# Kernel tuning notes

Hardware: AMD Instinct MI355X
Metric: run time of the kernel (lower is better)

Reference implementation:

```python
import jax, jax.numpy as jnp
import numpy as np

IM_H, IM_W = 240, 320
ENV_R, ENV_C = 120, 160
ENV_H, ENV_W = 8, 16
GRID = 8
NGRIDS = 6 * GRID * GRID  # 384


def _normalize(v, axis, eps=1e-6):
    return v / (jnp.linalg.norm(v, axis=axis, keepdims=True) + eps)


def setup_inputs() -> dict:
    key = jax.random.key(0)
    k1, k2, k3, k4 = jax.random.split(key, 4)
    B = 2
    normalPred = jax.random.normal(k1, (B, 3, IM_H, IM_W), dtype=jnp.float32)
    # positive depth in [0.5, 5.0] so z = -depth passes the z < -0.1 mask mostly
    depthPred = jax.random.uniform(k2, (B, IM_H, IM_W), dtype=jnp.float32, minval=0.5, maxval=5.0)
    envmapsPredImage = jax.random.uniform(k3, (B, 3, ENV_R, ENV_C, ENV_H, ENV_W), dtype=jnp.float32)
    # intrinsics must have cx = W/2, cy = H/2 (module asserts f_W_scale == f_H_scale)
    cam_K = jnp.tile(jnp.array([[300.0, 0.0, IM_W / 2.0],
                                [0.0, 300.0, IM_H / 2.0],
                                [0.0, 0.0, 1.0]], dtype=jnp.float32)[None], (B, 1, 1))
    # grid-cell centers of the 6 layout faces in LightNet coords (normally from get_grid_centers)
    verts_center_lightNet = jax.random.normal(k4, (B, 6, GRID, GRID, 3), dtype=jnp.float32) * 3.0
    return {"normalPred": normalPred, "depthPred": depthPred,
            "envmapsPredImage": envmapsPredImage, "cam_K": cam_K,
            "verts_center_lightNet": verts_center_lightNet}


def _forward(normalPred, depthPred, envmapsPredImage, cam_K, verts_center_lightNet):
    B = depthPred.shape[0]
    dt = depthPred.dtype
    # ---- back-project per-pixel 3D points from depth + intrinsics ----
    u0, v0 = IM_W / 2.0, IM_H / 2.0
    vv, uu = jnp.meshgrid(jnp.arange(IM_H, dtype=dt), jnp.arange(IM_W, dtype=dt), indexing='ij')
    f_pix = (cam_K[:, 0, 0] * (IM_W / 2.0) / cam_K[:, 0, 2]).reshape(B, 1, 1)
    z = -depthPred
    x = -(uu - u0) / f_pix * z
    y = (vv - v0) / f_pix * z
    points = jnp.stack([x, y, z], axis=1)  # [B,3,IM_H,IM_W]

    # ---- renderingLayer.forwardEnv (if_normal_only): per-pixel local frame at env res ----
    r = IM_H // ENV_R  # = IM_W // ENV_C = 2
    n = normalPred.reshape(B, 3, ENV_R, r, ENV_C, r).mean(axis=(3, 5))
    normal = _normalize(n, axis=1)                              # [B,3,eR,eC]
    up = jnp.array([0.0, 1.0, 0.0], dtype=dt).reshape(1, 3, 1, 1)
    camyProj = (up * normal).sum(axis=1, keepdims=True) * normal
    camy = _normalize(up - camyProj, axis=1)
    camx = -_normalize(jnp.cross(camy, normal, axis=1), axis=1)

    # ---- accu_light ----
    pts_s = points[:, :, ::r, ::r].transpose(0, 2, 3, 1)        # [B,eR,eC,3]
    mask = pts_s[..., 2] < -0.1                                 # [B,eR,eC]
    p_t = verts_center_lightNet.reshape(B, NGRIDS, 1, 1, 3)
    vec_to_t = p_t - pts_s[:, None]                             # [B,G,eR,eC,3]

    # A columns = [camx, camy, normal]; invert per pixel
    A = jnp.stack([camx.transpose(0, 2, 3, 1),
                   camy.transpose(0, 2, 3, 1),
                   normal.transpose(0, 2, 3, 1)], axis=-1)      # [B,eR,eC,3,3]
    A = A + 1e-6 * jnp.eye(3, dtype=dt)
    invA = jnp.linalg.inv(A)

    l_local = jnp.einsum('bhwij,bghwj->bghwi', invA, vec_to_t)  # [B,G,eR,eC,3]
    l_local = _normalize(l_local, axis=-1)
    cos_theta = l_local[..., 2]
    theta = jnp.arccos(cos_theta)
    sin_t = jnp.sin(theta) + 1e-6
    phi = jnp.arctan2(l_local[..., 1] / sin_t, l_local[..., 0] / sin_t)
    az = (phi / np.pi / 2.0 + 0.5) * ENV_W                      # [B,G,eR,eC]
    el = theta / np.pi * 2.0 * ENV_H

    # grid_sample(bilinear, padding='border', align_corners=False) on per-pixel 8x16 envmaps
    # normalized coord -> pixel coord: (uv/size*2-1 + 1)*size/2 - 0.5 = uv - 0.5
    az_f = jnp.clip(az.transpose(0, 2, 3, 1).reshape(-1, NGRIDS) - 0.5, 0.0, ENV_W - 1.0)
    el_f = jnp.clip(el.transpose(0, 2, 3, 1).reshape(-1, NGRIDS) - 0.5, 0.0, ENV_H - 1.0)
    x0 = jnp.floor(az_f); fx = az_f - x0
    y0 = jnp.floor(el_f); fy = el_f - y0
    x0i = x0.astype(jnp.int32); x1i = jnp.minimum(x0i + 1, ENV_W - 1)
    y0i = y0.astype(jnp.int32); y1i = jnp.minimum(y0i + 1, ENV_H - 1)

    env_flat = envmapsPredImage.transpose(0, 2, 3, 1, 4, 5).reshape(-1, 3, ENV_H * ENV_W)  # [Npix,3,128]

    def gather(yi, xi):
        idx = (yi * ENV_W + xi)[:, None, :]                     # [Npix,1,G]
        return jnp.take_along_axis(env_flat, idx, axis=2)       # [Npix,3,G]

    fx_ = fx[:, None, :]; fy_ = fy[:, None, :]
    val = (gather(y0i, x0i) * (1 - fx_) * (1 - fy_) +
           gather(y0i, x1i) * fx_ * (1 - fy_) +
           gather(y1i, x0i) * (1 - fx_) * fy_ +
           gather(y1i, x1i) * fx_ * fy_)                        # [Npix,3,G]

    env_acc = val.reshape(B, ENV_R, ENV_C, 3, NGRIDS).transpose(0, 3, 4, 1, 2)  # [B,3,G,eR,eC]
    mask_e = mask.astype(dt)[:, None, None]                     # [B,1,1,eR,eC]
    env_acc = env_acc * mask_e
    env_mean = (env_acc.sum((-1, -2)) / (mask_e.sum((-1, -2)) + 1e-6)).transpose(0, 2, 1)  # [B,G,3]
    return env_acc, env_mean, points, mask, vec_to_t


def reference(normalPred, depthPred, envmapsPredImage, cam_K, verts_center_lightNet):
    return _forward(normalPred, depthPred, envmapsPredImage, cam_K, verts_center_lightNet)
```

## Files before the change

kernel.cpp:

```cpp
#include <hip/hip_runtime.h>
#include <math.h>

namespace {

constexpr int IMH = 240, IMW = 320;
constexpr int ER = 120, EC = 160, EH = 8, EW = 16;
constexpr int NG = 384;
constexpr int NPIX = ER * EC;
constexpr int NB = 2;
constexpr int NTAP = EH * EW;

constexpr size_t ACC_N    = (size_t)NB * 3 * NG * NPIX;
constexpr size_t OFF_ACC  = 0;
constexpr size_t OFF_MEAN = OFF_ACC + ACC_N;
constexpr size_t MEAN_N   = (size_t)NB * NG * 3;
constexpr size_t OFF_PTS  = OFF_MEAN + MEAN_N;
constexpr size_t PTS_N    = (size_t)NB * 3 * IMH * IMW;
constexpr size_t OFF_MASK = OFF_PTS + PTS_N;
constexpr size_t MASK_N   = (size_t)NB * NPIX;
constexpr size_t OFF_VEC  = OFF_MASK + MASK_N;

constexpr int TPX   = 32;
constexpr int GLN   = 8;
constexpr int GIT   = NG / GLN;
constexpr int TILES = NPIX / TPX;
constexpr int LROW  = 132;

constexpr size_t WS_S     = (size_t)NB * NPIX;
constexpr size_t WS_INVA  = 0;
constexpr size_t WS_PTS   = WS_INVA + 9 * WS_S;
constexpr size_t WS_PART  = WS_PTS + 3 * WS_S;
constexpr size_t PART_N   = (size_t)NB * NG * 3 * TILES;
constexpr size_t WS_CNT_HI = WS_PART + PART_N;
constexpr size_t WS_CNT_LO = WS_PART;
constexpr size_t WS_NEED_HI = (WS_CNT_HI + NB) * 4;

__device__ __forceinline__ float fpix_of(const float* K, int b) {
    return K[b * 9 + 0] * (IMW * 0.5f) / K[b * 9 + 2];
}

__device__ __forceinline__ unsigned bf16r(float f) {
    unsigned b = __float_as_uint(f);
    return (b + 0x7FFFu + ((b >> 16) & 1u)) >> 16;
}
__device__ __forceinline__ float bfload(unsigned short u) {
    return __uint_as_float((unsigned)u << 16);
}

template <int CTRL, int RMASK>
__device__ __forceinline__ float dpp_add(float s) {
    int t = __builtin_amdgcn_update_dpp(0, __float_as_int(s), CTRL, RMASK, 0xf, true);
    return s + __int_as_float(t);
}
__device__ __forceinline__ float hw_sum(float s) {
    s = dpp_add<0x111, 0xf>(s);
    s = dpp_add<0x112, 0xf>(s);
    s = dpp_add<0x114, 0xf>(s);
    s = dpp_add<0x118, 0xf>(s);
    s = dpp_add<0x142, 0xa>(s);
    return s;
}

__device__ __forceinline__ float acos_el(float x) {
    float ax = fminf(fabsf(x), 1.0f);
    float p  = fmaf(fmaf(fmaf(-0.09538315f, ax, 0.37820512f), ax, -1.08021632f),
                    ax, 7.99996873f);
    float r  = sqrtf(1.0f - ax) * p;
    return (x >= 0.0f) ? r : 16.0f - r;
}

__device__ __forceinline__ float atan2_az(float y, float x) {
    float ay = fabsf(y), ax = fabsf(x);
    float mn = fminf(ax, ay), mx = fmaxf(ax, ay);
    float a  = mn * __builtin_amdgcn_rcpf(fmaxf(mx, 1e-37f));
    float s  = a * a;
    float r  = a * fmaf(s, fmaf(s, fmaf(s, fmaf(s, 0.05305631f, -0.21677864f),
                                        0.45872349f), -0.84104627f), 2.54613763f);
    if (ay > ax) r = 4.0f - r;
    if (x < 0.0f) r = 8.0f - r;
    return fmaf(copysignf(1.0f, y), r, 8.0f);
}

__global__ void k_points_zero(const float* __restrict__ depth,
                              const float* __restrict__ K,
                              float* __restrict__ out,
                              float* __restrict__ ws, size_t cnt_off) {
    int idx = blockIdx.x * 256 + threadIdx.x;
    if (blockIdx.x == 0 && threadIdx.x < NB) ws[cnt_off + threadIdx.x] = 0.0f;
    if (idx >= NB * IMH * IMW) return;
    int b  = idx / (IMH * IMW);
    int pp = idx - b * (IMH * IMW);
    int v  = pp / IMW;
    int u  = pp - v * IMW;
    float fp = fpix_of(K, b);
    float z  = -depth[idx];
    float x  = -(((float)u - IMW * 0.5f) / fp) * z;
    float y  =  (((float)v - IMH * 0.5f) / fp) * z;
    float* P = out + OFF_PTS + (size_t)b * 3 * IMH * IMW;
    P[pp]                 = x;
    P[pp + IMH * IMW]     = y;
    P[pp + 2 * IMH * IMW] = z;
}

__global__ void k_prep(const float* __restrict__ normal,
                       const float* __restrict__ depth,
                       const float* __restrict__ K,
                       float* __restrict__ out,
                       float* __restrict__ ws, size_t cnt_off) {
    int idx = blockIdx.x * 256 + threadIdx.x;
    if (idx >= NB * NPIX) return;
    int b   = idx / NPIX;
    int pix = idx - b * NPIX;
    int h   = pix / EC;
    int w   = pix - h * EC;
    int v = 2 * h, u = 2 * w;

    float fp = fpix_of(K, b);
    float z  = -depth[(size_t)b * IMH * IMW + (size_t)v * IMW + u];
    float px = -(((float)u - 160.0f) / fp) * z;
    float py =  (((float)v - 120.0f) / fp) * z;

    ws[WS_PTS + 0 * WS_S + idx] = px;
    ws[WS_PTS + 1 * WS_S + idx] = py;
    ws[WS_PTS + 2 * WS_S + idx] = z;

    float m = (z < -0.1f) ? 1.0f : 0.0f;
    out[OFF_MASK + idx] = m;
    float cm = m;
    for (int off = 32; off > 0; off >>= 1) cm += __shfl_down(cm, off);
    if ((threadIdx.x & 63) == 0) atomicAdd(&ws[cnt_off + b], cm);

    float n[3];
#pragma unroll
    for (int c = 0; c < 3; ++c) {
        const float* Nc = normal + ((size_t)(b * 3 + c) * IMH + v) * IMW + u;
        n[c] = 0.25f * (Nc[0] + Nc[1] + Nc[IMW] + Nc[IMW + 1]);
    }
    float nl = sqrtf(n[0]*n[0] + n[1]*n[1] + n[2]*n[2]) + 1e-6f;
    float nx = n[0] / nl, ny = n[1] / nl, nz = n[2] / nl;

    float t0 = -ny * nx, t1 = 1.0f - ny * ny, t2 = -ny * nz;
    float tl = sqrtf(t0*t0 + t1*t1 + t2*t2) + 1e-6f;
    float cy0 = t0 / tl, cy1 = t1 / tl, cy2 = t2 / tl;

    float cr0 = cy1 * nz - cy2 * ny;
    float cr1 = cy2 * nx - cy0 * nz;
    float cr2 = cy0 * ny - cy1 * nx;
    float cl = sqrtf(cr0*cr0 + cr1*cr1 + cr2*cr2) + 1e-6f;
    float cx0 = -cr0 / cl, cx1 = -cr1 / cl, cx2 = -cr2 / cl;

    float a00 = cx0 + 1e-6f, a01 = cy0,         a02 = nx;
    float a10 = cx1,         a11 = cy1 + 1e-6f, a12 = ny;
    float a20 = cx2,         a21 = cy2,         a22 = nz + 1e-6f;

    float c00 =  a11 * a22 - a12 * a21;
    float c01 = -(a10 * a22 - a12 * a20);
    float c02 =  a10 * a21 - a11 * a20;
    float det = a00 * c00 + a01 * c01 + a02 * c02;
    float id  = 1.0f / det;

    ws[WS_INVA + 0 * WS_S + idx] = c00 * id;
    ws[WS_INVA + 1 * WS_S + idx] = (a02 * a21 - a01 * a22) * id;
    ws[WS_INVA + 2 * WS_S + idx] = (a01 * a12 - a02 * a11) * id;
    ws[WS_INVA + 3 * WS_S + idx] = c01 * id;
    ws[WS_INVA + 4 * WS_S + idx] = (a00 * a22 - a02 * a20) * id;
    ws[WS_INVA + 5 * WS_S + idx] = (a02 * a10 - a00 * a12) * id;
    ws[WS_INVA + 6 * WS_S + idx] = c02 * id;
    ws[WS_INVA + 7 * WS_S + idx] = (a01 * a20 - a00 * a21) * id;
    ws[WS_INVA + 8 * WS_S + idx] = (a00 * a11 - a01 * a10) * id;
}

template <bool WP>
__global__ void __launch_bounds__(256) k_main(const float* __restrict__ env,
                       const float* __restrict__ verts,
                       float* __restrict__ out,
                       float* __restrict__ ws) {
    __shared__ unsigned       lds01[TPX * LROW];
    __shared__ unsigned short lds2 [TPX * LROW];

    int blk  = blockIdx.x;
    int b    = blk / TILES;
    int tile = blk - b * TILES;
    int px0  = tile * TPX;
    int t    = threadIdx.x;

    {
        const float* ebase = env + (size_t)b * 3 * NPIX * NTAP + (size_t)px0 * NTAP;
#pragma unroll
        for (int it2 = 0; it2 < 4; ++it2) {
            int idx2 = it2 * 256 + t;
            int ppx  = idx2 >> 5;
            int tq   = idx2 & 31;
            const float* p0 = ebase + (size_t)ppx * NTAP + tq * 4;
            float4 c0 = *(const float4*)(p0);
            float4 c1 = *(const float4*)(p0 + (size_t)NPIX * NTAP);
            float4 c2 = *(const float4*)(p0 + (size_t)2 * NPIX * NTAP);
            uint4 pk;
            pk.x = bf16r(c0.x) | (bf16r(c1.x) << 16);
            pk.y = bf16r(c0.y) | (bf16r(c1.y) << 16);
            pk.z = bf16r(c0.z) | (bf16r(c1.z) << 16);
            pk.w = bf16r(c0.w) | (bf16r(c1.w) << 16);
            *(uint4*)(&lds01[ppx * LROW + tq * 4]) = pk;
            ushort4 s4;
            s4.x = (unsigned short)bf16r(c2.x);
            s4.y = (unsigned short)bf16r(c2.y);
            s4.z = (unsigned short)bf16r(c2.z);
            s4.w = (unsigned short)bf16r(c2.w);
            *(ushort4*)(&lds2[ppx * LROW + tq * 4]) = s4;
        }
    }
    __syncthreads();

    int px_l  = t & 31;
    int glane = t >> 5;
    int pix   = px0 + px_l;
    int bp    = b * NPIX + pix;
    int row   = px_l * LROW;

    float px = ws[WS_PTS + 0 * WS_S + bp];
    float py = ws[WS_PTS + 1 * WS_S + bp];
    float pz = ws[WS_PTS + 2 * WS_S + bp];
    float i00 = ws[WS_INVA + 0 * WS_S + bp];
    float i01 = ws[WS_INVA + 1 * WS_S + bp];
    float i02 = ws[WS_INVA + 2 * WS_S + bp];
    float i10 = ws[WS_INVA + 3 * WS_S + bp];
    float i11 = ws[WS_INVA + 4 * WS_S + bp];
    float i12 = ws[WS_INVA + 5 * WS_S + bp];
    float i20 = ws[WS_INVA + 6 * WS_S + bp];
    float i21 = ws[WS_INVA + 7 * WS_S + bp];
    float i22 = ws[WS_INVA + 8 * WS_S + bp];
    float m = (pz < -0.1f) ? 1.0f : 0.0f;

    int g0 = glane * GIT;
    const float* vp = verts + ((size_t)b * NG + g0) * 3;
    float* pA0 = out + OFF_ACC + ((size_t)(b * 3 + 0) * NG + g0) * NPIX + pix;
    float* pA1 = out + OFF_ACC + ((size_t)(b * 3 + 1) * NG + g0) * NPIX + pix;
    float* pA2 = out + OFF_ACC + ((size_t)(b * 3 + 2) * NG + g0) * NPIX + pix;
    float* pV  = out + OFF_VEC + (((size_t)b * NG + g0) * NPIX + pix) * 3;
    float* pP  = ws + WS_PART + ((size_t)(b * NG + g0) * 3) * TILES + tile;

#pragma unroll 2
    for (int it = 0; it < GIT; ++it) {
        float vx = vp[0] - px, vy = vp[1] - py, vz = vp[2] - pz;
        pV[0] = vx; pV[1] = vy; pV[2] = vz;

        float l0 = i00 * vx + i01 * vy + i02 * vz;
        float l1 = i10 * vx + i11 * vy + i12 * vz;
        float l2 = i20 * vx + i21 * vy + i22 * vz;
        float nl = sqrtf(l0*l0 + l1*l1 + l2*l2) + 1e-6f;
        float l2n = l2 * __builtin_amdgcn_rcpf(nl);

        float el = acos_el(l2n);
        float az = atan2_az(l1, l0);

        float azf = __builtin_amdgcn_fmed3f(az - 0.5f, 0.0f, 15.0f);
        float elf = __builtin_amdgcn_fmed3f(el - 0.5f, 0.0f, 7.0f);
        float x0 = floorf(azf), y0 = floorf(elf);
        float fx = azf - x0,    fy = elf - y0;
        int x0i = (int)x0, y0i = (int)y0;
        int x1i = min(x0i + 1, 15);
        int y1i = min(y0i + 1, 7);

        float w00 = (1.0f - fx) * (1.0f - fy);
        float w01 = fx * (1.0f - fy);
        float w10 = (1.0f - fx) * fy;
        float w11 = fx * fy;

        int a00 = row + (y0i << 4) + x0i;
        int a01 = row + (y0i << 4) + x1i;
        int a10 = row + (y1i << 4) + x0i;
        int a11 = row + (y1i << 4) + x1i;

        unsigned q00 = lds01[a00], q01 = lds01[a01];
        unsigned q10 = lds01[a10], q11 = lds01[a11];

        float v0 = (__uint_as_float(q00 << 16) * w00 + __uint_as_float(q01 << 16) * w01 +
                    __uint_as_float(q10 << 16) * w10 + __uint_as_float(q11 << 16) * w11) * m;
        float v1 = (__uint_as_float(q00 & 0xFFFF0000u) * w00 + __uint_as_float(q01 & 0xFFFF0000u) * w01 +
                    __uint_as_float(q10 & 0xFFFF0000u) * w10 + __uint_as_float(q11 & 0xFFFF0000u) * w11) * m;
        float v2 = (bfload(lds2[a00]) * w00 + bfload(lds2[a01]) * w01 +
                    bfload(lds2[a10]) * w10 + bfload(lds2[a11]) * w11) * m;

        *pA0 = v0; *pA1 = v1; *pA2 = v2;

        if constexpr (WP) {
            float s0 = hw_sum(v0);
            float s1 = hw_sum(v1);
            float s2 = hw_sum(v2);
            if ((t & 31) == 31) {
                pP[0 * TILES] = s0;
                pP[1 * TILES] = s1;
                pP[2 * TILES] = s2;
            }
            pP += 3 * TILES;
        }

        vp  += 3;
        pV  += (size_t)NPIX * 3;
        pA0 += NPIX; pA1 += NPIX; pA2 += NPIX;
    }
}

__global__ void k_psum(float* __restrict__ out, const float* __restrict__ ws,
                       size_t cnt_off) {
    int r = blockIdx.x;
    int l = threadIdx.x;
    const float* p = ws + WS_PART + (size_t)r * TILES;
    float s = 0.0f;
    for (int i = l; i < TILES; i += 64) s += p[i];
#pragma unroll
    for (int off = 32; off > 0; off >>= 1) s += __shfl_down(s, off);
    if (l == 0) {
        int b = r / (NG * 3);
        out[OFF_MEAN + r] = s / (ws[cnt_off + b] + 1e-6f);
    }
}

__global__ void k_mean2(float* __restrict__ out, const float* __restrict__ ws,
                        size_t cnt_off) {
    __shared__ float wsum[4];
    int blk = blockIdx.x;
    int b   = blk / (3 * NG);
    int t   = threadIdx.x;

    const float4* r4 = (const float4*)(out + OFF_ACC + (size_t)blk * NPIX);
    float s = 0.0f;
    for (int i = t; i < NPIX / 4; i += 256) {
        float4 v = r4[i];
        s += v.x + v.y + v.z + v.w;
    }
    for (int off = 32; off > 0; off >>= 1) s += __shfl_down(s, off);
    if ((t & 63) == 0) wsum[t >> 6] = s;
    __syncthreads();
    if (t == 0) {
        int rc = blk - b * 3 * NG;
        int c  = rc / NG;
        int g  = rc - c * NG;
        float tot = wsum[0] + wsum[1] + wsum[2] + wsum[3];
        out[OFF_MEAN + ((size_t)b * NG + g) * 3 + c] = tot / (ws[cnt_off + b] + 1e-6f);
    }
}

}

extern "C" void kernel_launch(void* const* d_in, const int* in_sizes, int n_in,
                              void* d_out, int out_size, void* d_ws, size_t ws_size,
                              hipStream_t stream) {
    (void)in_sizes; (void)n_in; (void)out_size;
    const float* normalPred = (const float*)d_in[0];
    const float* depthPred  = (const float*)d_in[1];
    const float* env        = (const float*)d_in[2];
    const float* K          = (const float*)d_in[3];
    const float* verts      = (const float*)d_in[4];
    float* out = (float*)d_out;
    float* ws  = (float*)d_ws;

    const bool big = ws_size >= WS_NEED_HI;
    const size_t cnt_off = big ? WS_CNT_HI : WS_CNT_LO;

    k_points_zero<<<(NB * IMH * IMW + 255) / 256, 256, 0, stream>>>(depthPred, K, out, ws, cnt_off);
    k_prep<<<(NB * NPIX + 255) / 256, 256, 0, stream>>>(normalPred, depthPred, K, out, ws, cnt_off);
    if (big) {
        k_main<true><<<NB * TILES, 256, 0, stream>>>(env, verts, out, ws);
        k_psum<<<NB * NG * 3, 64, 0, stream>>>(out, ws, cnt_off);
    } else {
        k_main<false><<<NB * TILES, 256, 0, stream>>>(env, verts, out, ws);
        k_mean2<<<NB * 3 * NG, 256, 0, stream>>>(out, ws, cnt_off);
    }
}
```

Baseline: 125.1 us.

## Split vec_to_t output into separate coalesced float4 kernel and pad LDS rows

Moves the writing of the vec_to_t output out of the main env-sampling kernel into a dedicated kernel that writes contiguous float4 chunks. The old loop made strided 3-float scalar stores per pixel, which coalesce poorly. The LDS row stride for the packed channel-0/1 buffer also changes from 132 to 129 to cut bank conflicts during the random bilinear gathers. The cost is an extra launch and a second pass that re-reads points and verts, and the 129 stride forces scalar LDS writes in the staging phase.

```diff
diff --git a/kernel.cpp b/kernel.cpp
--- a/kernel.cpp
+++ b/kernel.cpp
@@ -24,7 +24,12 @@
 constexpr int GLN   = 8;
 constexpr int GIT   = NG / GLN;
 constexpr int TILES = NPIX / TPX;
-constexpr int LROW  = 132;
+constexpr int LR01  = 129;
+constexpr int LR2   = 132;
+
+constexpr int F4_PER_G = NPIX * 3 / 4;
+constexpr int F4_PER_B = NG * F4_PER_G;
+constexpr int VBLK     = NB * F4_PER_B / 1024;
 
 constexpr size_t WS_S     = (size_t)NB * NPIX;
 constexpr size_t WS_INVA  = 0;
@@ -170,13 +175,39 @@
     ws[WS_INVA + 8 * WS_S + idx] = (a00 * a11 - a01 * a10) * id;
 }
 
+__global__ void __launch_bounds__(256) k_vec(const float* __restrict__ verts,
+                                             float* __restrict__ out,
+                                             const float* __restrict__ ws) {
+#pragma unroll
+    for (int it = 0; it < 4; ++it) {
+        int f4i = (blockIdx.x * 4 + it) * 256 + threadIdx.x;
+        int b   = f4i / F4_PER_B;
+        int r4  = f4i - b * F4_PER_B;
+        int g   = r4 / F4_PER_G;
+        int rr  = (r4 - g * F4_PER_G) * 4;
+        const float* vv = verts + ((size_t)b * NG + g) * 3;
+        float v0 = vv[0], v1 = vv[1], v2 = vv[2];
+        const float* pb = ws + WS_PTS + (size_t)b * NPIX;
+        float4 o;
+#pragma unroll
+        for (int j = 0; j < 4; ++j) {
+            int rj  = rr + j;
+            int pxj = rj / 3;
+            int cj  = rj - 3 * pxj;
+            float vc = (cj == 0) ? v0 : ((cj == 1) ? v1 : v2);
+            (&o.x)[j] = vc - pb[(size_t)cj * WS_S + pxj];
+        }
+        *(float4*)(out + OFF_VEC + (size_t)f4i * 4) = o;
+    }
+}
+
 template <bool WP>
-__global__ void __launch_bounds__(256) k_main(const float* __restrict__ env,
+__global__ void __launch_bounds__(256) k_env(const float* __restrict__ env,
                        const float* __restrict__ verts,
                        float* __restrict__ out,
                        float* __restrict__ ws) {
-    __shared__ unsigned       lds01[TPX * LROW];
-    __shared__ unsigned short lds2 [TPX * LROW];
+    __shared__ unsigned       lds01[TPX * LR01];
+    __shared__ unsigned short lds2 [TPX * LR2];
 
     int blk  = blockIdx.x;
     int b    = blk / TILES;
@@ -195,18 +226,17 @@
             float4 c0 = *(const float4*)(p0);
             float4 c1 = *(const float4*)(p0 + (size_t)NPIX * NTAP);
             float4 c2 = *(const float4*)(p0 + (size_t)2 * NPIX * NTAP);
-            uint4 pk;
-            pk.x = bf16r(c0.x) | (bf16r(c1.x) << 16);
-            pk.y = bf16r(c0.y) | (bf16r(c1.y) << 16);
-            pk.z = bf16r(c0.z) | (bf16r(c1.z) << 16);
-            pk.w = bf16r(c0.w) | (bf16r(c1.w) << 16);
-            *(uint4*)(&lds01[ppx * LROW + tq * 4]) = pk;
+#pragma unroll
+            for (int k = 0; k < 4; ++k) {
+                lds01[ppx * LR01 + tq * 4 + k] =
+                    bf16r((&c0.x)[k]) | (bf16r((&c1.x)[k]) << 16);
+            }
             ushort4 s4;
             s4.x = (unsigned short)bf16r(c2.x);
             s4.y = (unsigned short)bf16r(c2.y);
             s4.z = (unsigned short)bf16r(c2.z);
             s4.w = (unsigned short)bf16r(c2.w);
-            *(ushort4*)(&lds2[ppx * LROW + tq * 4]) = s4;
+            *(ushort4*)(&lds2[ppx * LR2 + tq * 4]) = s4;
         }
     }
     __syncthreads();
@@ -215,7 +245,8 @@
     int glane = t >> 5;
     int pix   = px0 + px_l;
     int bp    = b * NPIX + pix;
-    int row   = px_l * LROW;
+    int row1  = px_l * LR01;
+    int row2  = px_l * LR2;
 
     float px = ws[WS_PTS + 0 * WS_S + bp];
     float py = ws[WS_PTS + 1 * WS_S + bp];
@@ -236,13 +267,11 @@
     float* pA0 = out + OFF_ACC + ((size_t)(b * 3 + 0) * NG + g0) * NPIX + pix;
     float* pA1 = out + OFF_ACC + ((size_t)(b * 3 + 1) * NG + g0) * NPIX + pix;
     float* pA2 = out + OFF_ACC + ((size_t)(b * 3 + 2) * NG + g0) * NPIX + pix;
-    float* pV  = out + OFF_VEC + (((size_t)b * NG + g0) * NPIX + pix) * 3;
     float* pP  = ws + WS_PART + ((size_t)(b * NG + g0) * 3) * TILES + tile;
 
 #pragma unroll 2
     for (int it = 0; it < GIT; ++it) {
         float vx = vp[0] - px, vy = vp[1] - py, vz = vp[2] - pz;
-        pV[0] = vx; pV[1] = vy; pV[2] = vz;
 
         float l0 = i00 * vx + i01 * vy + i02 * vz;
         float l1 = i10 * vx + i11 * vy + i12 * vz;
@@ -266,20 +295,20 @@
         float w10 = (1.0f - fx) * fy;
         float w11 = fx * fy;
 
-        int a00 = row + (y0i << 4) + x0i;
-        int a01 = row + (y0i << 4) + x1i;
-        int a10 = row + (y1i << 4) + x0i;
-        int a11 = row + (y1i << 4) + x1i;
-
-        unsigned q00 = lds01[a00], q01 = lds01[a01];
-        unsigned q10 = lds01[a10], q11 = lds01[a11];
+        int t00 = (y0i << 4) + x0i;
+        int t01 = (y0i << 4) + x1i;
+        int t10 = (y1i << 4) + x0i;
+        int t11 = (y1i << 4) + x1i;
+
+        unsigned q00 = lds01[row1 + t00], q01 = lds01[row1 + t01];
+        unsigned q10 = lds01[row1 + t10], q11 = lds01[row1 + t11];
 
         float v0 = (__uint_as_float(q00 << 16) * w00 + __uint_as_float(q01 << 16) * w01 +
                     __uint_as_float(q10 << 16) * w10 + __uint_as_float(q11 << 16) * w11) * m;
         float v1 = (__uint_as_float(q00 & 0xFFFF0000u) * w00 + __uint_as_float(q01 & 0xFFFF0000u) * w01 +
                     __uint_as_float(q10 & 0xFFFF0000u) * w10 + __uint_as_float(q11 & 0xFFFF0000u) * w11) * m;
-        float v2 = (bfload(lds2[a00]) * w00 + bfload(lds2[a01]) * w01 +
-                    bfload(lds2[a10]) * w10 + bfload(lds2[a11]) * w11) * m;
+        float v2 = (bfload(lds2[row2 + t00]) * w00 + bfload(lds2[row2 + t01]) * w01 +
+                    bfload(lds2[row2 + t10]) * w10 + bfload(lds2[row2 + t11]) * w11) * m;
 
         *pA0 = v0; *pA1 = v1; *pA2 = v2;
 
@@ -296,7 +325,6 @@
         }
 
         vp  += 3;
-        pV  += (size_t)NPIX * 3;
         pA0 += NPIX; pA1 += NPIX; pA2 += NPIX;
     }
 }
@@ -360,11 +388,12 @@
 
     k_points_zero<<<(NB * IMH * IMW + 255) / 256, 256, 0, stream>>>(depthPred, K, out, ws, cnt_off);
     k_prep<<<(NB * NPIX + 255) / 256, 256, 0, stream>>>(normalPred, depthPred, K, out, ws, cnt_off);
+    k_vec<<<VBLK, 256, 0, stream>>>(verts, out, ws);
     if (big) {
-        k_main<true><<<NB * TILES, 256, 0, stream>>>(env, verts, out, ws);
+        k_env<true><<<NB * TILES, 256, 0, stream>>>(env, verts, out, ws);
         k_psum<<<NB * NG * 3, 64, 0, stream>>>(out, ws, cnt_off);
     } else {
-        k_main<false><<<NB * TILES, 256, 0, stream>>>(env, verts, out, ws);
+        k_env<false><<<NB * TILES, 256, 0, stream>>>(env, verts, out, ws);
         k_mean2<<<NB * 3 * NG, 256, 0, stream>>>(out, ws, cnt_off);
     }
 }
```

After: 170.1 us. 35.9% more time.
